# Optimization experiments

Measured on AMD Instinct MI355X. Metric: run time of the kernel, lower is better.

The kernel has to match this reference:

```python
import jax, jax.numpy as jnp
import numpy as np

D_MODEL = 1024
N_HEADS = 16
HEAD_DIM = D_MODEL // N_HEADS


def setup_inputs() -> dict:
    key = jax.random.key(0)
    k1, k2, k3 = jax.random.split(key, 3)
    B, T = 4, 2048
    x = jax.random.normal(k1, (B, T, D_MODEL), dtype=jnp.float32)
    # match nn.Linear default init scale roughly (small weights for stability)
    w_qkv = jax.random.normal(k2, (D_MODEL, 3 * D_MODEL), dtype=jnp.float32) / np.sqrt(D_MODEL)
    w_proj = jax.random.normal(k3, (D_MODEL, D_MODEL), dtype=jnp.float32) / np.sqrt(D_MODEL)
    b_proj = jnp.zeros((D_MODEL,), dtype=jnp.float32)
    return {"x": x, "w_qkv": w_qkv, "w_proj": w_proj, "b_proj": b_proj}


def reference(x, w_qkv, w_proj, b_proj):
    B, T, C = x.shape
    qkv = x @ w_qkv  # [B,T,3C]
    q, k, v = jnp.split(qkv, 3, axis=-1)
    # [B, H, T, hd]
    q = q.reshape(B, T, N_HEADS, HEAD_DIM).transpose(0, 2, 1, 3)
    k = k.reshape(B, T, N_HEADS, HEAD_DIM).transpose(0, 2, 1, 3)
    v = v.reshape(B, T, N_HEADS, HEAD_DIM).transpose(0, 2, 1, 3)
    scale = 1.0 / np.sqrt(HEAD_DIM).astype(np.float32)
    att = jnp.einsum("bhqd,bhkd->bhqk", q, k) * scale
    causal = jnp.tril(jnp.ones((T, T), dtype=bool))
    att = jnp.where(causal[None, None], att, jnp.float32(-jnp.inf))
    att = jax.nn.softmax(att, axis=-1)
    # dropout p=0.0 (eval) -> identity
    out = jnp.einsum("bhqk,bhkd->bhqd", att, v)
    out = out.transpose(0, 2, 1, 3).reshape(B, T, C)
    return out @ w_proj + b_proj
```

## Files before the change

### kernel.cpp

```cpp
#include <hip/hip_runtime.h>
#include <stdint.h>

#define D_MODEL 1024
#define N_HEADS 16
#define HEAD_DIM 64
#define BATCH 4
#define SEQ 2048
#define ROWS (BATCH * SEQ)
#define K3 (3 * D_MODEL)
#define NQT (SEQ / 64)
#define SCALE_Q 0.1803368867f

typedef unsigned short u16;
typedef unsigned int u32;
typedef __attribute__((ext_vector_type(8))) short short8;
typedef __attribute__((ext_vector_type(4))) float floatx4;

typedef const __attribute__((address_space(1))) u32* gptr_t;
typedef __attribute__((address_space(3))) u32* lptr_t;

__device__ __forceinline__ float bf2f(u16 u) {
    return __uint_as_float(((unsigned)u) << 16);
}
__device__ __forceinline__ u16 f2b(float f) {
    unsigned u = __float_as_uint(f);
    u = u + 0x7fffu + ((u >> 16) & 1u);
    return (u16)(u >> 16);
}
__device__ __forceinline__ unsigned pk2(float a, float b) {
    return (unsigned)f2b(a) | ((unsigned)f2b(b) << 16);
}

__global__ __launch_bounds__(256) void conv_f2b4(const float* __restrict__ x,
                                                 u16* __restrict__ xb, int n4) {
    int i = blockIdx.x * 256 + threadIdx.x;
    if (i < n4) {
        float4 v = ((const float4*)x)[i];
        uint2 p;
        p.x = pk2(v.x, v.y);
        p.y = pk2(v.z, v.w);
        ((uint2*)xb)[i] = p;
    }
}

__global__ __launch_bounds__(256) void transpose_f2b_t(const float* __restrict__ w,
                                                       u16* __restrict__ wt,
                                                       int R, int C) {
    __shared__ u16 tile[64][65];
    const int tx = threadIdx.x & 63;
    const int ty = threadIdx.x >> 6;
    const int r0 = blockIdx.y * 64, c0 = blockIdx.x * 64;
    #pragma unroll
    for (int i = 0; i < 16; ++i) {
        const int r = i * 4 + ty;
        tile[r][tx] = f2b(w[(size_t)(r0 + r) * C + c0 + tx]);
    }
    __syncthreads();
    #pragma unroll
    for (int i = 0; i < 16; ++i) {
        const int c = i * 4 + ty;
        wt[(size_t)(c0 + c) * R + r0 + tx] = tile[tx][c];
    }
}

__global__ __launch_bounds__(256) void transpose_v2(const u16* __restrict__ v,
                                                    u16* __restrict__ vt) {
    __shared__ u16 tile[64][65];
    const int bh = blockIdx.y;
    const int t0 = blockIdx.x * 64;
    const int tx = threadIdx.x & 63, ty = threadIdx.x >> 6;
    const u16* src = v + ((size_t)bh * SEQ + t0) * HEAD_DIM;
    #pragma unroll
    for (int i = 0; i < 16; ++i) {
        const int r = i * 4 + ty;
        tile[r][tx] = src[r * HEAD_DIM + tx];
    }
    __syncthreads();
    u16* dst = vt + (size_t)bh * HEAD_DIM * SEQ + t0;
    #pragma unroll
    for (int i = 0; i < 16; ++i) {
        const int d = i * 4 + ty;
        dst[(size_t)d * SEQ + tx] = tile[tx][d];
    }
}

#define GEMM_CORE_GLD(KDIM)                                                    \
    __shared__ u16 As[128][64];                                                \
    __shared__ u16 Bs[128][64];                                                \
    const int tid  = threadIdx.x;                                              \
    const int wave = tid >> 6, lane = tid & 63;                                \
    const int quad = lane >> 4, l15 = lane & 15;                               \
    const int wr = wave >> 1, wc = wave & 1;                                   \
    const int m0 = blockIdx.y * 128, n0 = blockIdx.x * 128;                    \
    const int lrow8 = lane >> 3;                                               \
    const int csw = 8 * ((lane & 7) ^ lrow8);           \
    const int swA = (l15 & 7) * 8;                      \
    floatx4 acc[4][4] = {};                                                    \
    for (int k0 = 0; k0 < (KDIM); k0 += 64) {                                  \
        _Pragma("unroll")                                                      \
        for (int i = 0; i < 4; ++i) {                                          \
            const int rb = i * 32 + wave * 8;                                  \
            const int r  = rb + lrow8;                                         \
            __builtin_amdgcn_global_load_lds(                                  \
                (gptr_t)(A + (size_t)(m0 + r) * (KDIM) + k0 + csw),            \
                (lptr_t)(&As[rb][0]), 16, 0, 0);                               \
            __builtin_amdgcn_global_load_lds(                                  \
                (gptr_t)(Bt + (size_t)(n0 + r) * (KDIM) + k0 + csw),           \
                (lptr_t)(&Bs[rb][0]), 16, 0, 0);                               \
        }                                                                      \
        __syncthreads();                                                       \
        _Pragma("unroll")                                                      \
        for (int ks = 0; ks < 2; ++ks) {                                       \
            const int kk = ks * 32 + quad * 8;                                 \
            short8 af[4], bf[4];                                               \
            _Pragma("unroll")                                                  \
            for (int t = 0; t < 4; ++t) {                                      \
                af[t] = *(const short8*)&As[wr * 64 + t * 16 + l15][kk ^ swA]; \
                bf[t] = *(const short8*)&Bs[wc * 64 + t * 16 + l15][kk ^ swA]; \
            }                                                                  \
            _Pragma("unroll")                                                  \
            for (int i = 0; i < 4; ++i)                                        \
                _Pragma("unroll")                                              \
                for (int j = 0; j < 4; ++j)                                    \
                    acc[i][j] = __builtin_amdgcn_mfma_f32_16x16x32_bf16(       \
                        af[i], bf[j], acc[i][j], 0, 0, 0);                     \
        }                                                                      \
        __syncthreads();                                                       \
    }

__global__ __launch_bounds__(256) void gemm_qkv(const u16* __restrict__ A,
                                                const u16* __restrict__ Bt,
                                                u16* __restrict__ qo,
                                                u16* __restrict__ ko,
                                                u16* __restrict__ vo) {
    GEMM_CORE_GLD(D_MODEL)
    const int which = n0 >> 10;
    u16* dst = which == 0 ? qo : (which == 1 ? ko : vo);
    const float scl = which == 0 ? SCALE_Q : 1.f;
    #pragma unroll
    for (int i = 0; i < 4; ++i)
        #pragma unroll
        for (int j = 0; j < 4; ++j) {
            const int col = n0 + wc * 64 + j * 16 + l15;
            const int rb  = m0 + wr * 64 + i * 16 + quad * 4;
            const int cc  = col & 1023;
            const int h = cc >> 6, d = cc & 63;
            #pragma unroll
            for (int rr = 0; rr < 4; ++rr) {
                const int row = rb + rr;
                const int b = row >> 11, t = row & 2047;
                dst[(((size_t)(b * N_HEADS + h)) * SEQ + t) * HEAD_DIM + d] =
                    f2b(acc[i][j][rr] * scl);
            }
        }
}

__global__ __launch_bounds__(256) void gemm_proj(const u16* __restrict__ A,
                                                 const u16* __restrict__ Bt,
                                                 const float* __restrict__ bias,
                                                 float* __restrict__ out) {
    GEMM_CORE_GLD(D_MODEL)
    #pragma unroll
    for (int i = 0; i < 4; ++i)
        #pragma unroll
        for (int j = 0; j < 4; ++j) {
            const int col = n0 + wc * 64 + j * 16 + l15;
            const int rb  = m0 + wr * 64 + i * 16 + quad * 4;
            const float bv = bias[col];
            #pragma unroll
            for (int rr = 0; rr < 4; ++rr) {
                const int row = rb + rr;
                out[(size_t)row * D_MODEL + col] = acc[i][j][rr] + bv;
            }
        }
}

__global__ __launch_bounds__(256, 4) void attn_mfma(const u16* __restrict__ q,
                                                    const u16* __restrict__ k,
                                                    const u16* __restrict__ vt,
                                                    u16* __restrict__ o) {
    __shared__ u16 Ks[2][64][64];
    __shared__ u16 Vs[2][64][64];
    __shared__ u16 Plds[4][16][64];
    const int tid = threadIdx.x;
    const int w = tid >> 6, lane = tid & 63;
    const int quad = lane >> 4, l15 = lane & 15;
    const int bh = blockIdx.y;
    const int b = bh >> 4, h = bh & 15;
    const u16* kb  = k  + (size_t)bh * SEQ * HEAD_DIM;
    const u16* vtb = vt + (size_t)bh * HEAD_DIM * SEQ;
    const int lrow8 = lane >> 3;
    const int csw = 8 * ((lane & 7) ^ lrow8);
    const int swA = (l15 & 7) * 8;
    const int r0 = w * 16 + lrow8;

    #pragma unroll 1
    for (int seg = 0; seg < 2; ++seg) {
        const int qt = seg ? (int)blockIdx.x : (NQT - 1 - (int)blockIdx.x);
        const int qrow = qt * 64 + w * 16 + l15;
        const u16* qp = q + ((size_t)bh * SEQ + qrow) * HEAD_DIM + quad * 8;
        const short8 bq0 = *(const short8*)(qp);
        const short8 bq1 = *(const short8*)(qp + 32);

        floatx4 O[4] = {};
        float l = 0.f;

        __syncthreads();
        __builtin_amdgcn_global_load_lds(
            (gptr_t)(kb + (size_t)(r0) * HEAD_DIM + csw),
            (lptr_t)(&Ks[0][w * 16][0]), 16, 0, 0);
        __builtin_amdgcn_global_load_lds(
            (gptr_t)(kb + (size_t)(r0 + 8) * HEAD_DIM + csw),
            (lptr_t)(&Ks[0][w * 16 + 8][0]), 16, 0, 0);
        __builtin_amdgcn_global_load_lds(
            (gptr_t)(vtb + (size_t)(r0) * SEQ + csw),
            (lptr_t)(&Vs[0][w * 16][0]), 16, 0, 0);
        __builtin_amdgcn_global_load_lds(
            (gptr_t)(vtb + (size_t)(r0 + 8) * SEQ + csw),
            (lptr_t)(&Vs[0][w * 16 + 8][0]), 16, 0, 0);

        for (int c = 0; c <= qt; ++c) {
            const int cb = c & 1;
            __syncthreads();
            if (c < qt) {
                const int nb = cb ^ 1;
                __builtin_amdgcn_global_load_lds(
                    (gptr_t)(kb + (size_t)((c + 1) * 64 + r0) * HEAD_DIM + csw),
                    (lptr_t)(&Ks[nb][w * 16][0]), 16, 0, 0);
                __builtin_amdgcn_global_load_lds(
                    (gptr_t)(kb + (size_t)((c + 1) * 64 + r0 + 8) * HEAD_DIM + csw),
                    (lptr_t)(&Ks[nb][w * 16 + 8][0]), 16, 0, 0);
                __builtin_amdgcn_global_load_lds(
                    (gptr_t)(vtb + (size_t)(r0) * SEQ + (c + 1) * 64 + csw),
                    (lptr_t)(&Vs[nb][w * 16][0]), 16, 0, 0);
                __builtin_amdgcn_global_load_lds(
                    (gptr_t)(vtb + (size_t)(r0 + 8) * SEQ + (c + 1) * 64 + csw),
                    (lptr_t)(&Vs[nb][w * 16 + 8][0]), 16, 0, 0);
            }
            floatx4 s[4];
            #pragma unroll
            for (int kt = 0; kt < 4; ++kt) {
                short8 ak0 = *(const short8*)&Ks[cb][kt * 16 + l15][(quad * 8) ^ swA];
                short8 ak1 = *(const short8*)&Ks[cb][kt * 16 + l15][(32 + quad * 8) ^ swA];
                floatx4 z = {};
                z = __builtin_amdgcn_mfma_f32_16x16x32_bf16(ak0, bq0, z, 0, 0, 0);
                z = __builtin_amdgcn_mfma_f32_16x16x32_bf16(ak1, bq1, z, 0, 0, 0);
                s[kt] = z;
            }
            float e[4][4];
            #pragma unroll
            for (int kt = 0; kt < 4; ++kt)
                #pragma unroll
                for (int r = 0; r < 4; ++r)
                    e[kt][r] = exp2f(s[kt][r]);
            if (c == qt) {
                #pragma unroll
                for (int kt = 0; kt < 4; ++kt)
                    #pragma unroll
                    for (int r = 0; r < 4; ++r)
                        if (kt * 16 + quad * 4 + r > w * 16 + l15) e[kt][r] = 0.f;
            }
            float ls = 0.f;
            #pragma unroll
            for (int kt = 0; kt < 4; ++kt) {
                ls += (e[kt][0] + e[kt][1]) + (e[kt][2] + e[kt][3]);
                uint2 pkv;
                pkv.x = pk2(e[kt][0], e[kt][1]);
                pkv.y = pk2(e[kt][2], e[kt][3]);
                *(uint2*)&Plds[w][l15][(kt * 16 + quad * 4) ^ swA] = pkv;
            }
            l += ls;
            short8 pb0 = *(const short8*)&Plds[w][l15][(quad * 8) ^ swA];
            short8 pb1 = *(const short8*)&Plds[w][l15][(32 + quad * 8) ^ swA];
            #pragma unroll
            for (int dt = 0; dt < 4; ++dt) {
                short8 av0 = *(const short8*)&Vs[cb][dt * 16 + l15][(quad * 8) ^ swA];
                short8 av1 = *(const short8*)&Vs[cb][dt * 16 + l15][(32 + quad * 8) ^ swA];
                O[dt] = __builtin_amdgcn_mfma_f32_16x16x32_bf16(av0, pb0, O[dt], 0, 0, 0);
                O[dt] = __builtin_amdgcn_mfma_f32_16x16x32_bf16(av1, pb1, O[dt], 0, 0, 0);
            }
        }
        l += __shfl_xor(l, 16);
        l += __shfl_xor(l, 32);
        const float inv = 1.f / l;
        u16* op = o + ((size_t)(b * SEQ + qrow)) * D_MODEL + h * 64 + quad * 4;
        #pragma unroll
        for (int dt = 0; dt < 4; ++dt) {
            uint2 pkv;
            pkv.x = pk2(O[dt][0] * inv, O[dt][1] * inv);
            pkv.y = pk2(O[dt][2] * inv, O[dt][3] * inv);
            *(uint2*)(op + dt * 16) = pkv;
        }
    }
}

extern "C" void kernel_launch(void* const* d_in, const int* in_sizes, int n_in,
                              void* d_out, int out_size, void* d_ws, size_t ws_size,
                              hipStream_t stream) {
    const float* x      = (const float*)d_in[0];
    const float* w_qkv  = (const float*)d_in[1];
    const float* w_proj = (const float*)d_in[2];
    const float* b_proj = (const float*)d_in[3];
    float* out = (float*)d_out;

    u16* xb      = (u16*)d_ws;
    u16* wt_qkv  = xb + (size_t)ROWS * D_MODEL;
    u16* wt_proj = wt_qkv + (size_t)D_MODEL * K3;
    u16* qws     = wt_proj + (size_t)D_MODEL * D_MODEL;
    u16* kws     = qws + (size_t)ROWS * D_MODEL;
    u16* vtws    = kws + (size_t)ROWS * D_MODEL;
    u16* aout    = vtws + (size_t)ROWS * D_MODEL;
    u16* vnat    = aout;

    conv_f2b4<<<(ROWS * D_MODEL / 4 + 255) / 256, 256, 0, stream>>>(x, xb, ROWS * D_MODEL / 4);
    transpose_f2b_t<<<dim3(K3 / 64, D_MODEL / 64), 256, 0, stream>>>(w_qkv, wt_qkv, D_MODEL, K3);
    transpose_f2b_t<<<dim3(D_MODEL / 64, D_MODEL / 64), 256, 0, stream>>>(w_proj, wt_proj, D_MODEL, D_MODEL);

    gemm_qkv<<<dim3(K3 / 128, ROWS / 128), 256, 0, stream>>>(xb, wt_qkv, qws, kws, vnat);

    transpose_v2<<<dim3(SEQ / 64, BATCH * N_HEADS), 256, 0, stream>>>(vnat, vtws);

    attn_mfma<<<dim3(NQT / 2, BATCH * N_HEADS), 256, 0, stream>>>(qws, kws, vtws, aout);

    gemm_proj<<<dim3(D_MODEL / 128, ROWS / 128), 256, 0, stream>>>(aout, wt_proj, b_proj, out);
}
```

Measured before the change: 272.3 us.

## Split paired causal attention tiles into one block per tile, single-buffer LDS

The attention kernel no longer processes a pair of query tiles per block. It launches one block per query tile, heaviest tiles first, and drops the K/V double buffering so LDS use falls and more blocks (launch bound 6) fit per CU. Load overlap now comes from occupancy instead of in-block prefetch, with an extra barrier per chunk. It also uses the raw hardware exp2 builtin and a cheaper round-half-up bf16 pack via byte permute, which slightly changes rounding on ties.

```diff
diff --git a/kernel.cpp b/kernel.cpp
--- a/kernel.cpp
+++ b/kernel.cpp
@@ -19,6 +19,12 @@
 typedef const __attribute__((address_space(1))) u32* gptr_t;
 typedef __attribute__((address_space(3))) u32* lptr_t;
 
+#if __has_builtin(__builtin_amdgcn_exp2f)
+#define EXP2(x) __builtin_amdgcn_exp2f(x)
+#else
+#define EXP2(x) exp2f(x)
+#endif
+
 __device__ __forceinline__ float bf2f(u16 u) {
     return __uint_as_float(((unsigned)u) << 16);
 }
@@ -29,6 +35,14 @@
 }
 __device__ __forceinline__ unsigned pk2(float a, float b) {
     return (unsigned)f2b(a) | ((unsigned)f2b(b) << 16);
+}
+__device__ __forceinline__ unsigned pk2r(float a, float b) {
+#if __has_builtin(__builtin_amdgcn_perm)
+    return __builtin_amdgcn_perm(__float_as_uint(b) + 0x8000u,
+                                 __float_as_uint(a) + 0x8000u, 0x07060302u);
+#else
+    return pk2(a, b);
+#endif
 }
 
 __global__ __launch_bounds__(256) void conv_f2b4(const float* __restrict__ x,
@@ -37,8 +51,8 @@
     if (i < n4) {
         float4 v = ((const float4*)x)[i];
         uint2 p;
-        p.x = pk2(v.x, v.y);
-        p.y = pk2(v.z, v.w);
+        p.x = pk2r(v.x, v.y);
+        p.y = pk2r(v.z, v.w);
         ((uint2*)xb)[i] = p;
     }
 }
@@ -175,18 +189,19 @@
         }
 }
 
-__global__ __launch_bounds__(256, 4) void attn_mfma(const u16* __restrict__ q,
+__global__ __launch_bounds__(256, 6) void attn_mfma(const u16* __restrict__ q,
                                                     const u16* __restrict__ k,
                                                     const u16* __restrict__ vt,
                                                     u16* __restrict__ o) {
-    __shared__ u16 Ks[2][64][64];
-    __shared__ u16 Vs[2][64][64];
+    __shared__ u16 Ks[64][64];
+    __shared__ u16 Vs[64][64];
     __shared__ u16 Plds[4][16][64];
     const int tid = threadIdx.x;
     const int w = tid >> 6, lane = tid & 63;
     const int quad = lane >> 4, l15 = lane & 15;
     const int bh = blockIdx.y;
     const int b = bh >> 4, h = bh & 15;
+    const int qt = NQT - 1 - (int)blockIdx.x;
     const u16* kb  = k  + (size_t)bh * SEQ * HEAD_DIM;
     const u16* vtb = vt + (size_t)bh * HEAD_DIM * SEQ;
     const int lrow8 = lane >> 3;
@@ -194,103 +209,82 @@
     const int swA = (l15 & 7) * 8;
     const int r0 = w * 16 + lrow8;
 
-    #pragma unroll 1
-    for (int seg = 0; seg < 2; ++seg) {
-        const int qt = seg ? (int)blockIdx.x : (NQT - 1 - (int)blockIdx.x);
-        const int qrow = qt * 64 + w * 16 + l15;
-        const u16* qp = q + ((size_t)bh * SEQ + qrow) * HEAD_DIM + quad * 8;
-        const short8 bq0 = *(const short8*)(qp);
-        const short8 bq1 = *(const short8*)(qp + 32);
-
-        floatx4 O[4] = {};
-        float l = 0.f;
-
+    const int qrow = qt * 64 + w * 16 + l15;
+    const u16* qp = q + ((size_t)bh * SEQ + qrow) * HEAD_DIM + quad * 8;
+    const short8 bq0 = *(const short8*)(qp);
+    const short8 bq1 = *(const short8*)(qp + 32);
+
+    floatx4 O[4] = {};
+    float l = 0.f;
+
+    for (int c = 0; c <= qt; ++c) {
         __syncthreads();
         __builtin_amdgcn_global_load_lds(
-            (gptr_t)(kb + (size_t)(r0) * HEAD_DIM + csw),
-            (lptr_t)(&Ks[0][w * 16][0]), 16, 0, 0);
+            (gptr_t)(kb + (size_t)(c * 64 + r0) * HEAD_DIM + csw),
+            (lptr_t)(&Ks[w * 16][0]), 16, 0, 0);
         __builtin_amdgcn_global_load_lds(
-            (gptr_t)(kb + (size_t)(r0 + 8) * HEAD_DIM + csw),
-            (lptr_t)(&Ks[0][w * 16 + 8][0]), 16, 0, 0);
+            (gptr_t)(kb + (size_t)(c * 64 + r0 + 8) * HEAD_DIM + csw),
+            (lptr_t)(&Ks[w * 16 + 8][0]), 16, 0, 0);
         __builtin_amdgcn_global_load_lds(
-            (gptr_t)(vtb + (size_t)(r0) * SEQ + csw),
-            (lptr_t)(&Vs[0][w * 16][0]), 16, 0, 0);
+            (gptr_t)(vtb + (size_t)(r0) * SEQ + c * 64 + csw),
+            (lptr_t)(&Vs[w * 16][0]), 16, 0, 0);
         __builtin_amdgcn_global_load_lds(
-            (gptr_t)(vtb + (size_t)(r0 + 8) * SEQ + csw),
-            (lptr_t)(&Vs[0][w * 16 + 8][0]), 16, 0, 0);
-
-        for (int c = 0; c <= qt; ++c) {
-            const int cb = c & 1;
-            __syncthreads();
-            if (c < qt) {
-                const int nb = cb ^ 1;
-                __builtin_amdgcn_global_load_lds(
-                    (gptr_t)(kb + (size_t)((c + 1) * 64 + r0) * HEAD_DIM + csw),
-                    (lptr_t)(&Ks[nb][w * 16][0]), 16, 0, 0);
-                __builtin_amdgcn_global_load_lds(
-                    (gptr_t)(kb + (size_t)((c + 1) * 64 + r0 + 8) * HEAD_DIM + csw),
-                    (lptr_t)(&Ks[nb][w * 16 + 8][0]), 16, 0, 0);
-                __builtin_amdgcn_global_load_lds(
-                    (gptr_t)(vtb + (size_t)(r0) * SEQ + (c + 1) * 64 + csw),
-                    (lptr_t)(&Vs[nb][w * 16][0]), 16, 0, 0);
-                __builtin_amdgcn_global_load_lds(
-                    (gptr_t)(vtb + (size_t)(r0 + 8) * SEQ + (c + 1) * 64 + csw),
-                    (lptr_t)(&Vs[nb][w * 16 + 8][0]), 16, 0, 0);
-            }
-            floatx4 s[4];
+            (gptr_t)(vtb + (size_t)(r0 + 8) * SEQ + c * 64 + csw),
+            (lptr_t)(&Vs[w * 16 + 8][0]), 16, 0, 0);
+        __syncthreads();
+        floatx4 s[4];
+        #pragma unroll
+        for (int kt = 0; kt < 4; ++kt) {
+            short8 ak0 = *(const short8*)&Ks[kt * 16 + l15][(quad * 8) ^ swA];
+            short8 ak1 = *(const short8*)&Ks[kt * 16 + l15][(32 + quad * 8) ^ swA];
+            floatx4 z = {};
+            z = __builtin_amdgcn_mfma_f32_16x16x32_bf16(ak0, bq0, z, 0, 0, 0);
+            z = __builtin_amdgcn_mfma_f32_16x16x32_bf16(ak1, bq1, z, 0, 0, 0);
+            s[kt] = z;
+        }
+        float e[4][4];
+        #pragma unroll
+        for (int kt = 0; kt < 4; ++kt)
             #pragma unroll
-            for (int kt = 0; kt < 4; ++kt) {
-                short8 ak0 = *(const short8*)&Ks[cb][kt * 16 + l15][(quad * 8) ^ swA];
-                short8 ak1 = *(const short8*)&Ks[cb][kt * 16 + l15][(32 + quad * 8) ^ swA];
-                floatx4 z = {};
-                z = __builtin_amdgcn_mfma_f32_16x16x32_bf16(ak0, bq0, z, 0, 0, 0);
-                z = __builtin_amdgcn_mfma_f32_16x16x32_bf16(ak1, bq1, z, 0, 0, 0);
-                s[kt] = z;
-            }
-            float e[4][4];
+            for (int r = 0; r < 4; ++r)
+                e[kt][r] = EXP2(s[kt][r]);
+        if (c == qt) {
             #pragma unroll
             for (int kt = 0; kt < 4; ++kt)
                 #pragma unroll
                 for (int r = 0; r < 4; ++r)
-                    e[kt][r] = exp2f(s[kt][r]);
-            if (c == qt) {
-                #pragma unroll
-                for (int kt = 0; kt < 4; ++kt)
-                    #pragma unroll
-                    for (int r = 0; r < 4; ++r)
-                        if (kt * 16 + quad * 4 + r > w * 16 + l15) e[kt][r] = 0.f;
-            }
-            float ls = 0.f;
-            #pragma unroll
-            for (int kt = 0; kt < 4; ++kt) {
-                ls += (e[kt][0] + e[kt][1]) + (e[kt][2] + e[kt][3]);
-                uint2 pkv;
-                pkv.x = pk2(e[kt][0], e[kt][1]);
-                pkv.y = pk2(e[kt][2], e[kt][3]);
-                *(uint2*)&Plds[w][l15][(kt * 16 + quad * 4) ^ swA] = pkv;
-            }
-            l += ls;
-            short8 pb0 = *(const short8*)&Plds[w][l15][(quad * 8) ^ swA];
-            short8 pb1 = *(const short8*)&Plds[w][l15][(32 + quad * 8) ^ swA];
-            #pragma unroll
-            for (int dt = 0; dt < 4; ++dt) {
-                short8 av0 = *(const short8*)&Vs[cb][dt * 16 + l15][(quad * 8) ^ swA];
-                short8 av1 = *(const short8*)&Vs[cb][dt * 16 + l15][(32 + quad * 8) ^ swA];
-                O[dt] = __builtin_amdgcn_mfma_f32_16x16x32_bf16(av0, pb0, O[dt], 0, 0, 0);
-                O[dt] = __builtin_amdgcn_mfma_f32_16x16x32_bf16(av1, pb1, O[dt], 0, 0, 0);
-            }
-        }
-        l += __shfl_xor(l, 16);
-        l += __shfl_xor(l, 32);
-        const float inv = 1.f / l;
-        u16* op = o + ((size_t)(b * SEQ + qrow)) * D_MODEL + h * 64 + quad * 4;
+                    if (kt * 16 + quad * 4 + r > w * 16 + l15) e[kt][r] = 0.f;
+        }
+        float ls = 0.f;
+        #pragma unroll
+        for (int kt = 0; kt < 4; ++kt) {
+            ls += (e[kt][0] + e[kt][1]) + (e[kt][2] + e[kt][3]);
+            uint2 pkv;
+            pkv.x = pk2r(e[kt][0], e[kt][1]);
+            pkv.y = pk2r(e[kt][2], e[kt][3]);
+            *(uint2*)&Plds[w][l15][(kt * 16 + quad * 4) ^ swA] = pkv;
+        }
+        l += ls;
+        short8 pb0 = *(const short8*)&Plds[w][l15][(quad * 8) ^ swA];
+        short8 pb1 = *(const short8*)&Plds[w][l15][(32 + quad * 8) ^ swA];
         #pragma unroll
         for (int dt = 0; dt < 4; ++dt) {
-            uint2 pkv;
-            pkv.x = pk2(O[dt][0] * inv, O[dt][1] * inv);
-            pkv.y = pk2(O[dt][2] * inv, O[dt][3] * inv);
-            *(uint2*)(op + dt * 16) = pkv;
-        }
+            short8 av0 = *(const short8*)&Vs[dt * 16 + l15][(quad * 8) ^ swA];
+            short8 av1 = *(const short8*)&Vs[dt * 16 + l15][(32 + quad * 8) ^ swA];
+            O[dt] = __builtin_amdgcn_mfma_f32_16x16x32_bf16(av0, pb0, O[dt], 0, 0, 0);
+            O[dt] = __builtin_amdgcn_mfma_f32_16x16x32_bf16(av1, pb1, O[dt], 0, 0, 0);
+        }
+    }
+    l += __shfl_xor(l, 16);
+    l += __shfl_xor(l, 32);
+    const float inv = 1.f / l;
+    u16* op = o + ((size_t)(b * SEQ + qrow)) * D_MODEL + h * 64 + quad * 4;
+    #pragma unroll
+    for (int dt = 0; dt < 4; ++dt) {
+        uint2 pkv;
+        pkv.x = pk2r(O[dt][0] * inv, O[dt][1] * inv);
+        pkv.y = pk2r(O[dt][2] * inv, O[dt][3] * inv);
+        *(uint2*)(op + dt * 16) = pkv;
     }
 }
 
@@ -320,7 +314,7 @@
 
     transpose_v2<<<dim3(SEQ / 64, BATCH * N_HEADS), 256, 0, stream>>>(vnat, vtws);
 
-    attn_mfma<<<dim3(NQT / 2, BATCH * N_HEADS), 256, 0, stream>>>(qws, kws, vtws, aout);
+    attn_mfma<<<dim3(NQT, BATCH * N_HEADS), 256, 0, stream>>>(qws, kws, vtws, aout);
 
     gemm_proj<<<dim3(D_MODEL / 128, ROWS / 128), 256, 0, stream>>>(aout, wt_proj, b_proj, out);
 }
```

New measurement: 288.8 us. +6.1%, slower.
